# Optimization experiments

Hardware: AMD Instinct MI355X
Metric: run time of the kernel (lower is better)

Reference implementation:

```python
import jax, jax.numpy as jnp
import numpy as np

B, H, W, C = 16, 64, 64, 256
NH = 8          # num_heads
WS = 8          # window size (8,8) from shift=2
HID = 1024      # mlp hidden = 4*C
EPS = 1e-5


def _rel_index():
    # relative_position_index exactly as in the torch module (meshgrid 'ij')
    ch = np.arange(WS)
    coords = np.stack(np.meshgrid(ch, ch, indexing='ij'))          # (2, WS, WS)
    flat = coords.reshape(2, -1)                                    # (2, N)
    rel = flat[:, :, None] - flat[:, None, :]                       # (2, N, N)
    rel = rel.transpose(1, 2, 0).astype(np.int64)                   # (N, N, 2)
    rel[..., 0] += WS - 1
    rel[..., 1] += WS - 1
    rel[..., 0] *= 2 * WS - 1
    return jnp.asarray(rel.sum(-1))                                 # (N, N)


def _ln(x, w, b):
    m = x.mean(-1, keepdims=True)
    v = jnp.mean((x - m) ** 2, axis=-1, keepdims=True)
    return (x - m) / jnp.sqrt(v + EPS) * w + b


def setup_inputs() -> dict:
    key = jax.random.key(0)
    ks = jax.random.split(key, 16)
    std = 0.02
    n_bias = (2 * WS - 1) * (2 * WS - 1)  # 225
    return {
        'x': jax.random.normal(ks[0], (B, H * W, C), jnp.float32),
        'norm1_w': jnp.ones((C,), jnp.float32),
        'norm1_b': jnp.zeros((C,), jnp.float32),
        'qkv_w': jax.random.normal(ks[1], (3 * C, C), jnp.float32) * std,
        'qkv_b': jnp.zeros((3 * C,), jnp.float32),
        'rel_bias': jax.random.normal(ks[2], (n_bias, NH), jnp.float32) * std,
        'proj_w': jax.random.normal(ks[3], (C, C), jnp.float32) * std,
        'proj_b': jnp.zeros((C,), jnp.float32),
        'norm2_w': jnp.ones((C,), jnp.float32),
        'norm2_b': jnp.zeros((C,), jnp.float32),
        'fc1_w': jax.random.normal(ks[4], (HID, C), jnp.float32) * std,
        'fc1_b': jnp.zeros((HID,), jnp.float32),
        'dw_w': jax.random.normal(ks[5], (3, 3, 1, HID), jnp.float32) * std,  # HWIO depthwise
        'dw_b': jnp.zeros((HID,), jnp.float32),
        'fc2_w': jax.random.normal(ks[6], (C, HID), jnp.float32) * std,
        'fc2_b': jnp.zeros((C,), jnp.float32),
    }


def reference(x, norm1_w, norm1_b, qkv_w, qkv_b, rel_bias, proj_w, proj_b,
              norm2_w, norm2_b, fc1_w, fc1_b, dw_w, dw_b, fc2_w, fc2_b):
    S = (H // WS) * (W // WS)   # num windows = 64
    N = WS * WS                 # tokens per window = 64
    shortcut = x
    h = _ln(x, norm1_w, norm1_b).reshape(B, H, W, C)
    # window partition -> (B, S, N, C), then permute to (B, N, S, C)
    hw = (h.reshape(B, H // WS, WS, W // WS, WS, C)
            .transpose(0, 1, 3, 2, 4, 5)
            .reshape(B, S, N, C))
    xw = hw.transpose(0, 2, 1, 3)            # (B, N, S, C)
    # qkv over flattened (N*S) tokens; heads split the S*C feature dim
    xf = xw.reshape(B, N * S, C)
    qkv = xf @ qkv_w.T + qkv_b               # (B, N*S, 3C)
    qkv = qkv.reshape(B, N, 3, NH, S * C // NH).transpose(2, 0, 3, 1, 4)
    q, k, v = qkv[0], qkv[1], qkv[2]         # (B, NH, N, S*C/NH)
    scale = (C // NH) ** -0.5
    attn = jnp.einsum('bhnd,bhmd->bhnm', q, k) * scale   # (B, NH, N, N)
    idx = _rel_index()
    bias = rel_bias[idx.reshape(-1)].reshape(N, N, NH).transpose(2, 0, 1)
    attn = jax.nn.softmax(attn + bias[None], axis=-1)
    out = jnp.einsum('bhnm,bhmd->bhnd', attn, v)         # (B, NH, N, S*C/NH)
    out = out.transpose(0, 2, 1, 3).reshape(B, N * S, C)
    out = (out @ proj_w.T + proj_b).reshape(B, N, S, C).transpose(0, 2, 1, 3)  # (B,S,N,C)
    # window reverse -> (B, H*W, C)
    xr = (out.reshape(B, H // WS, W // WS, WS, WS, C)
             .transpose(0, 1, 3, 2, 4, 5)
             .reshape(B, H * W, C))
    x = shortcut + xr
    # conv-based MLP (eval mode, dropout = identity)
    y = _ln(x, norm2_w, norm2_b).reshape(B, H, H, C)      # NHWC
    y = jnp.einsum('bhwc,oc->bhwo', y, fc1_w) + fc1_b     # 1x1 conv
    y = jax.lax.conv_general_dilated(
        y, dw_w, (1, 1), 'SAME',
        dimension_numbers=('NHWC', 'HWIO', 'NHWC'),
        feature_group_count=HID) + dw_b
    y = jax.nn.gelu(y, approximate=False)
    y = jnp.einsum('bhwo,co->bhwc', y, fc2_w) + fc2_b     # 1x1 conv
    return x + y.reshape(B, H * W, C)
```

## Files before the change

kernel.cpp:

```cpp
#include <hip/hip_runtime.h>
#include <hip/hip_bf16.h>
#include <cstdint>
#include <cstddef>

#define B_     16
#define HW_    4096
#define C_     256
#define NH_    8
#define S_     64
#define N_     64
#define C3_    768
#define HID_   1024
#define DHEAD_ 2048
#define EPS_   1e-5f

using u16 = unsigned short;
using u32 = unsigned int;

typedef __attribute__((ext_vector_type(8))) short bf16x8;
typedef __attribute__((ext_vector_type(4))) float f32x4;

__device__ __forceinline__ float bf2f(u16 u) {
  union { float f; u32 i; } x; x.i = ((u32)u) << 16; return x.f;
}
__device__ __forceinline__ u16 f2bf(float f) {
  union { float f; u32 i; } x; x.f = f;
  u32 r = (x.i + 0x7FFFu + ((x.i >> 16) & 1u)) >> 16;
  return (u16)r;
}

__device__ __forceinline__ void gload_lds16(const u16* g, u16* l) {
  __builtin_amdgcn_global_load_lds(
      (const __attribute__((address_space(1))) unsigned int*)g,
      (__attribute__((address_space(3))) unsigned int*)l, 16, 0, 0);
}

__launch_bounds__(256)
__global__ void pack_w_kernel(const float* __restrict__ W, u16* __restrict__ out,
                              int K, int kshift) {
  int g = blockIdx.x * 256 + threadIdx.x;
  int lane = g & 63;
  int pk = g >> 6;
  int cb = pk >> kshift;
  int kb = pk & ((1 << kshift) - 1);
  int j = cb * 16 + (lane & 15);
  int k = kb * 32 + ((lane >> 4) << 3);
  const float* src = W + (size_t)j * K + k;
  float4 a = ((const float4*)src)[0];
  float4 b = ((const float4*)src)[1];
  ushort4 lo = {f2bf(a.x), f2bf(a.y), f2bf(a.z), f2bf(a.w)};
  ushort4 hi = {f2bf(b.x), f2bf(b.y), f2bf(b.z), f2bf(b.w)};
  ushort4* dst = (ushort4*)(out + (size_t)g * 8);
  dst[0] = lo;
  dst[1] = hi;
}

__launch_bounds__(256)
__global__ void ln_kernel(const float* __restrict__ in, const float* __restrict__ w,
                          const float* __restrict__ bias, u16* __restrict__ out,
                          int b_base) {
  int wave = threadIdx.x >> 6;
  int lane = threadIdx.x & 63;
  int t = blockIdx.x * 4 + wave;
  int b = b_base + (t >> 12);
  int r = t & 4095;
  int n = r >> 6, s = r & 63;
  int hw = (((s >> 3) << 3) + (n >> 3)) * 64 + ((s & 7) << 3) + (n & 7);
  size_t src_row = ((size_t)b << 12) + hw;
  float4 v = ((const float4*)(in + src_row * C_))[lane];
  float sum = v.x + v.y + v.z + v.w;
#pragma unroll
  for (int off = 32; off; off >>= 1) sum += __shfl_xor(sum, off);
  float mean = sum * (1.0f / C_);
  float4 d = {v.x - mean, v.y - mean, v.z - mean, v.w - mean};
  float ss = d.x * d.x + d.y * d.y + d.z * d.z + d.w * d.w;
#pragma unroll
  for (int off = 32; off; off >>= 1) ss += __shfl_xor(ss, off);
  float rstd = rsqrtf(ss * (1.0f / C_) + EPS_);
  float4 w4 = ((const float4*)w)[lane];
  float4 b4 = ((const float4*)bias)[lane];
  ushort4 o;
  o.x = f2bf(d.x * rstd * w4.x + b4.x);
  o.y = f2bf(d.y * rstd * w4.y + b4.y);
  o.z = f2bf(d.z * rstd * w4.z + b4.z);
  o.w = f2bf(d.w * rstd * w4.w + b4.w);
  ((ushort4*)(out + (size_t)t * C_))[lane] = o;
}

template<int K_, int J_, int EPI>
__launch_bounds__(256)
__global__ void gemm_mfma(const u16* __restrict__ A, const u16* __restrict__ wpk,
                          const float* __restrict__ bias, u16* __restrict__ outB,
                          float* __restrict__ outF, const float* __restrict__ res,
                          int m_base, u16* __restrict__ qb, u16* __restrict__ kb,
                          u16* __restrict__ vt) {
  constexpr int NT = K_ / 64;
  __shared__ u16 As[2][128 * 64];
  int tid = threadIdx.x;
  int wid = tid >> 6, lane = tid & 63;
  int n0 = blockIdx.x * 128;
  int m0 = blockIdx.y * 128;
  int wr = wid >> 1, wc = wid & 1;
  f32x4 acc[4][4] = {};
  int srow8 = lane >> 3, sslot = lane & 7;

#define ASTAGE(buf, t)                                                         \
  {                                                                            \
    int k0g = (t) * 64;                                                        \
    int cbb = ((sslot ^ srow8) << 4);                                          \
    _Pragma("unroll")                                                          \
    for (int r = 0; r < 4; ++r) {                                              \
      int row = wid * 32 + r * 8 + srow8;                                      \
      gload_lds16(A + (size_t)(m0 + row) * K_ + k0g + (cbb >> 1),              \
                  &As[buf][(wid * 32 + r * 8) * 64]);                          \
    }                                                                          \
  }

  ASTAGE(0, 0);
  asm volatile("s_waitcnt vmcnt(0)" ::: "memory");
  __builtin_amdgcn_sched_barrier(0);
  __builtin_amdgcn_s_barrier();
  __builtin_amdgcn_sched_barrier(0);

  for (int t = 0; t < NT; ++t) {
    bf16x8 bfr[8];
#pragma unroll
    for (int kk = 0; kk < 2; ++kk)
#pragma unroll
      for (int nf = 0; nf < 4; ++nf)
        bfr[kk * 4 + nf] = *(const bf16x8*)&wpk[
            ((size_t)(((n0 >> 4) + wc * 4 + nf) * (K_ / 32) + (t * 2 + kk)) * 64 + lane) * 8];
    if (t + 1 < NT) ASTAGE((t + 1) & 1, t + 1);
    const u16* as = As[t & 1];
#pragma unroll
    for (int kk = 0; kk < 2; ++kk) {
      bf16x8 afr[4];
#pragma unroll
      for (int mf = 0; mf < 4; ++mf) {
        int ra = wr * 64 + mf * 16 + (lane & 15);
        int cbb = (((kk * 4 + (lane >> 4)) ^ (ra & 7)) << 4);
        afr[mf] = *(const bf16x8*)&as[ra * 64 + (cbb >> 1)];
      }
#pragma unroll
      for (int mf = 0; mf < 4; ++mf)
#pragma unroll
        for (int nf = 0; nf < 4; ++nf)
          acc[mf][nf] = __builtin_amdgcn_mfma_f32_16x16x32_bf16(afr[mf], bfr[kk * 4 + nf], acc[mf][nf], 0, 0, 0);
    }
    asm volatile("s_waitcnt vmcnt(0)" ::: "memory");
    __builtin_amdgcn_sched_barrier(0);
    __builtin_amdgcn_s_barrier();
    __builtin_amdgcn_sched_barrier(0);
  }
#undef ASTAGE

#pragma unroll
  for (int nf = 0; nf < 4; ++nf) {
    int col = n0 + wc * 64 + nf * 16 + (lane & 15);
    float bv = bias[col];
#pragma unroll
    for (int mf = 0; mf < 4; ++mf) {
#pragma unroll
      for (int j = 0; j < 4; ++j) {
        int m = m0 + wr * 64 + mf * 16 + (lane >> 4) * 4 + j;
        float v = acc[mf][nf][j] + bv;
        if (EPI == 0) {
          outB[(size_t)m * J_ + col] = f2bf(v);
        } else if (EPI == 2) {
          size_t o = (size_t)(m_base + m) * C_ + col;
          outF[o] += v;
        } else {
          int b_rel = m >> 12, nn = (m >> 6) & 63, s = m & 63;
          int f = s * 768 + col;
          int part = f >> 14, hh = (f >> 11) & 7, d = f & 2047;
          u16 val = f2bf(v);
          size_t bh = (size_t)b_rel * 8 + hh;
          if (part == 0)      qb[(bh * 64 + nn) * 2048 + d] = val;
          else if (part == 1) kb[(bh * 64 + nn) * 2048 + d] = val;
          else                vt[(bh * 2048 + d) * 64 + nn] = val;
        }
      }
    }
  }
}

__launch_bounds__(256)
__global__ void proj_ln_fused(const u16* __restrict__ A, const u16* __restrict__ wpk,
                              const float* __restrict__ bias, const float* __restrict__ res,
                              float* __restrict__ outF, const float* __restrict__ ln_w,
                              const float* __restrict__ ln_b, u16* __restrict__ h2,
                              int m_base) {
  __shared__ u16 As[2][64 * 64];
  __shared__ float red[64][8];
  int tid = threadIdx.x;
  int wid = tid >> 6, lane = tid & 63;
  int m0 = blockIdx.x * 64;
  f32x4 acc[4][4] = {};
  int srow8 = lane >> 3, sslot = lane & 7;

#define PSTAGE(buf, t)                                                         \
  {                                                                            \
    int k0g = (t) * 64;                                                        \
    int cbb = ((sslot ^ srow8) << 4);                                          \
    _Pragma("unroll")                                                          \
    for (int r = 0; r < 2; ++r) {                                              \
      int row = wid * 16 + r * 8 + srow8;                                      \
      gload_lds16(A + (size_t)(m0 + row) * 256 + k0g + (cbb >> 1),             \
                  &As[buf][(wid * 16 + r * 8) * 64]);                          \
    }                                                                          \
  }

  PSTAGE(0, 0);
  asm volatile("s_waitcnt vmcnt(0)" ::: "memory");
  __builtin_amdgcn_sched_barrier(0);
  __builtin_amdgcn_s_barrier();
  __builtin_amdgcn_sched_barrier(0);

#pragma unroll
  for (int t = 0; t < 4; ++t) {
    bf16x8 bfr[8];
#pragma unroll
    for (int kk = 0; kk < 2; ++kk)
#pragma unroll
      for (int nf = 0; nf < 4; ++nf)
        bfr[kk * 4 + nf] = *(const bf16x8*)&wpk[
            ((size_t)((wid * 4 + nf) * 8 + (t * 2 + kk)) * 64 + lane) * 8];
    if (t + 1 < 4) PSTAGE((t + 1) & 1, t + 1);
    const u16* as = As[t & 1];
#pragma unroll
    for (int kk = 0; kk < 2; ++kk) {
      bf16x8 afr[4];
#pragma unroll
      for (int mf = 0; mf < 4; ++mf) {
        int ra = mf * 16 + (lane & 15);
        int cbb = (((kk * 4 + (lane >> 4)) ^ (ra & 7)) << 4);
        afr[mf] = *(const bf16x8*)&as[ra * 64 + (cbb >> 1)];
      }
#pragma unroll
      for (int mf = 0; mf < 4; ++mf)
#pragma unroll
        for (int nf = 0; nf < 4; ++nf)
          acc[mf][nf] = __builtin_amdgcn_mfma_f32_16x16x32_bf16(afr[mf], bfr[kk * 4 + nf], acc[mf][nf], 0, 0, 0);
    }
    asm volatile("s_waitcnt vmcnt(0)" ::: "memory");
    __builtin_amdgcn_sched_barrier(0);
    __builtin_amdgcn_s_barrier();
    __builtin_amdgcn_sched_barrier(0);
  }
#undef PSTAGE

#pragma unroll
  for (int mf = 0; mf < 4; ++mf) {
#pragma unroll
    for (int j = 0; j < 4; ++j) {
      int m = m0 + mf * 16 + (lane >> 4) * 4 + j;
      int gm = m_base + m;
      int b = gm >> 12, nn = (gm >> 6) & 63, s = gm & 63;
      int hw = (((s >> 3) << 3) + (nn >> 3)) * 64 + ((s & 7) << 3) + (nn & 7);
      size_t rowo = (((size_t)b << 12) + hw) * C_;
      float s1 = 0.f, s2 = 0.f;
#pragma unroll
      for (int nf = 0; nf < 4; ++nf) {
        int col = wid * 64 + nf * 16 + (lane & 15);
        float v = acc[mf][nf][j] + bias[col] + res[rowo + col];
        acc[mf][nf][j] = v;
        outF[rowo + col] = v;
        s1 += v; s2 += v * v;
      }
#pragma unroll
      for (int off = 1; off < 16; off <<= 1) {
        s1 += __shfl_xor(s1, off);
        s2 += __shfl_xor(s2, off);
      }
      if ((lane & 15) == 0) {
        int rr = mf * 16 + (lane >> 4) * 4 + j;
        red[rr][wid * 2] = s1;
        red[rr][wid * 2 + 1] = s2;
      }
    }
  }
  __syncthreads();

#pragma unroll
  for (int mf = 0; mf < 4; ++mf) {
#pragma unroll
    for (int j = 0; j < 4; ++j) {
      int rr = mf * 16 + (lane >> 4) * 4 + j;
      float sum = red[rr][0] + red[rr][2] + red[rr][4] + red[rr][6];
      float ssq = red[rr][1] + red[rr][3] + red[rr][5] + red[rr][7];
      float mean = sum * (1.0f / C_);
      float var = ssq * (1.0f / C_) - mean * mean;
      float rstd = rsqrtf(var + EPS_);
      int m = m0 + rr;
      int b_rel = m >> 12, nn = (m >> 6) & 63, s = m & 63;
      int hw = (((s >> 3) << 3) + (nn >> 3)) * 64 + ((s & 7) << 3) + (nn & 7);
      size_t ho = (((size_t)b_rel << 12) + hw) * C_;
#pragma unroll
      for (int nf = 0; nf < 4; ++nf) {
        int col = wid * 64 + nf * 16 + (lane & 15);
        float nv = (acc[mf][nf][j] - mean) * rstd * ln_w[col] + ln_b[col];
        h2[ho + col] = f2bf(nv);
      }
    }
  }
}

__launch_bounds__(256)
__global__ void attn_mfma(const u16* __restrict__ qb, const u16* __restrict__ kb,
                          const u16* __restrict__ vt, const float* __restrict__ rel_bias,
                          u16* __restrict__ outp) {
  __shared__ u16 bufA[4096];
  __shared__ u16 bufB[4096];
  int bh = blockIdx.x;
  int h = bh & 7;
  int b_rel = bh >> 3;
  int tid = threadIdx.x;
  int w = tid >> 6, lane = tid & 63;
  int l3 = lane >> 3, l7 = lane & 7;
  const u16* qg = qb + (size_t)bh * 64 * 2048;
  const u16* kg = kb + (size_t)bh * 64 * 2048;
  const u16* vg = vt + (size_t)bh * 2048 * 64;

  f32x4 acc[4] = {};
  for (int k0 = 0; k0 < 2048; k0 += 64) {
#pragma unroll
    for (int r = 0; r < 2; ++r) {
      int row = w * 16 + r * 8 + l3;
      int sc = (l7 ^ (row & 7)) * 8;
      gload_lds16(qg + (size_t)row * 2048 + k0 + sc, &bufA[(w * 16 + r * 8) * 64]);
      gload_lds16(kg + (size_t)row * 2048 + k0 + sc, &bufB[(w * 16 + r * 8) * 64]);
    }
    __syncthreads();
    int rowq = w * 16 + (lane & 15);
#pragma unroll
    for (int ks = 0; ks < 2; ++ks) {
      bf16x8 aq = *(const bf16x8*)&bufA[rowq * 64 + (((ks * 4 + (lane >> 4)) ^ (rowq & 7)) << 3)];
#pragma unroll
      for (int cf = 0; cf < 4; ++cf) {
        int m = cf * 16 + (lane & 15);
        bf16x8 bk = *(const bf16x8*)&bufB[m * 64 + (((ks * 4 + (lane >> 4)) ^ (m & 7)) << 3)];
        acc[cf] = __builtin_amdgcn_mfma_f32_16x16x32_bf16(aq, bk, acc[cf], 0, 0, 0);
      }
    }
    __syncthreads();
  }

  const float scale = 0.17677669529663688f;
#pragma unroll
  for (int j = 0; j < 4; ++j) {
    int r = w * 16 + (lane >> 4) * 4 + j;
    int i1 = r >> 3, j1 = r & 7;
    float v[4];
#pragma unroll
    for (int cf = 0; cf < 4; ++cf) {
      int c = cf * 16 + (lane & 15);
      int idx = (i1 - (c >> 3) + 7) * 15 + (j1 - (c & 7) + 7);
      v[cf] = acc[cf][j] * scale + rel_bias[idx * NH_ + h];
    }
    float mx = fmaxf(fmaxf(v[0], v[1]), fmaxf(v[2], v[3]));
#pragma unroll
    for (int off = 8; off; off >>= 1) mx = fmaxf(mx, __shfl_xor(mx, off));
    float sm = 0.f;
#pragma unroll
    for (int cf = 0; cf < 4; ++cf) { v[cf] = __expf(v[cf] - mx); sm += v[cf]; }
#pragma unroll
    for (int off = 8; off; off >>= 1) sm += __shfl_xor(sm, off);
    float inv = 1.0f / sm;
#pragma unroll
    for (int cf = 0; cf < 4; ++cf) {
      int c = cf * 16 + (lane & 15);
      bufA[r * 64 + (c ^ ((r & 7) << 3))] = f2bf(v[cf] * inv);
    }
  }
  __syncthreads();

  bf16x8 pa[2];
  {
    int n = w * 16 + (lane & 15);
#pragma unroll
    for (int ks = 0; ks < 2; ++ks)
      pa[ks] = *(const bf16x8*)&bufA[n * 64 + ((ks * 32 + (lane >> 4) * 8) ^ ((n & 7) << 3))];
  }

  for (int d0 = 0; d0 < 2048; d0 += 64) {
#pragma unroll
    for (int r = 0; r < 2; ++r) {
      int drow = w * 16 + r * 8 + l3;
      int sc = (l7 ^ (drow & 7)) * 8;
      gload_lds16(vg + (size_t)(d0 + drow) * 64 + sc, &bufB[(w * 16 + r * 8) * 64]);
    }
    __syncthreads();
    f32x4 o[4] = {};
#pragma unroll
    for (int ks = 0; ks < 2; ++ks)
#pragma unroll
      for (int cf = 0; cf < 4; ++cf) {
        int d = cf * 16 + (lane & 15);
        bf16x8 bv = *(const bf16x8*)&bufB[d * 64 + (((ks * 4 + (lane >> 4)) ^ (d & 7)) << 3)];
        o[cf] = __builtin_amdgcn_mfma_f32_16x16x32_bf16(pa[ks], bv, o[cf], 0, 0, 0);
      }
#pragma unroll
    for (int cf = 0; cf < 4; ++cf) {
      int f = h * 2048 + d0 + cf * 16 + (lane & 15);
      int s = f >> 8, c = f & 255;
#pragma unroll
      for (int j = 0; j < 4; ++j) {
        int n = w * 16 + (lane >> 4) * 4 + j;
        outp[(((size_t)b_rel * 64 + n) * 64 + s) * 256 + c] = f2bf(o[cf][j]);
      }
    }
    __syncthreads();
  }
}

__launch_bounds__(256)
__global__ void dwconv_gelu(const u16* __restrict__ y1, const float* __restrict__ dw_w,
                            const float* __restrict__ dw_b, u16* __restrict__ y2) {
  int bid = blockIdx.x;
  int wt = bid & 31, ht = (bid >> 5) & 15, b = bid >> 9;
  int h0 = ht * 4, w0 = wt * 2;
  int c0 = threadIdx.x * 4;

  float4 wv[9];
#pragma unroll
  for (int i = 0; i < 9; ++i) wv[i] = *(const float4*)&dw_w[i * HID_ + c0];

  ushort4 in[6][4];
#pragma unroll
  for (int ii = 0; ii < 6; ++ii) {
    int hh = h0 + ii - 1;
#pragma unroll
    for (int jj = 0; jj < 4; ++jj) {
      int ww = w0 + jj - 1;
      if ((unsigned)hh < 64u && (unsigned)ww < 64u)
        in[ii][jj] = *(const ushort4*)(y1 + ((size_t)((b << 12) + hh * 64 + ww)) * HID_ + c0);
      else
        in[ii][jj] = ushort4{0, 0, 0, 0};
    }
  }

  float4 bv = *(const float4*)&dw_b[c0];
  float4 acc[4][2];
#pragma unroll
  for (int i = 0; i < 4; ++i)
#pragma unroll
    for (int j = 0; j < 2; ++j) acc[i][j] = bv;

#pragma unroll
  for (int ii = 0; ii < 6; ++ii) {
#pragma unroll
    for (int jj = 0; jj < 4; ++jj) {
      ushort4 u = in[ii][jj];
      float4 f = {bf2f(u.x), bf2f(u.y), bf2f(u.z), bf2f(u.w)};
#pragma unroll
      for (int kh = 0; kh < 3; ++kh) {
        int i = ii - kh;
        if (i < 0 || i > 3) continue;
#pragma unroll
        for (int kw = 0; kw < 3; ++kw) {
          int j = jj - kw;
          if (j < 0 || j > 1) continue;
          float4 w4 = wv[kh * 3 + kw];
          acc[i][j].x += f.x * w4.x;
          acc[i][j].y += f.y * w4.y;
          acc[i][j].z += f.z * w4.z;
          acc[i][j].w += f.w * w4.w;
        }
      }
    }
  }

  const float k = 0.70710678118654752f;
#pragma unroll
  for (int i = 0; i < 4; ++i) {
#pragma unroll
    for (int j = 0; j < 2; ++j) {
      float4 a = acc[i][j];
      ushort4 o;
      o.x = f2bf(0.5f * a.x * (1.0f + erff(a.x * k)));
      o.y = f2bf(0.5f * a.y * (1.0f + erff(a.y * k)));
      o.z = f2bf(0.5f * a.z * (1.0f + erff(a.z * k)));
      o.w = f2bf(0.5f * a.w * (1.0f + erff(a.w * k)));
      *(ushort4*)(y2 + ((size_t)((b << 12) + (h0 + i) * 64 + (w0 + j))) * HID_ + c0) = o;
    }
  }
}

extern "C" void kernel_launch(void* const* d_in, const int* in_sizes, int n_in,
                              void* d_out, int out_size, void* d_ws, size_t ws_size,
                              hipStream_t stream) {
  const float* x       = (const float*)d_in[0];
  const float* norm1_w = (const float*)d_in[1];
  const float* norm1_b = (const float*)d_in[2];
  const float* qkv_w   = (const float*)d_in[3];
  const float* qkv_b   = (const float*)d_in[4];
  const float* rel_b   = (const float*)d_in[5];
  const float* proj_w  = (const float*)d_in[6];
  const float* proj_b  = (const float*)d_in[7];
  const float* norm2_w = (const float*)d_in[8];
  const float* norm2_b = (const float*)d_in[9];
  const float* fc1_w   = (const float*)d_in[10];
  const float* fc1_b   = (const float*)d_in[11];
  const float* dw_w    = (const float*)d_in[12];
  const float* dw_b    = (const float*)d_in[13];
  const float* fc2_w   = (const float*)d_in[14];
  const float* fc2_b   = (const float*)d_in[15];
  float* out = (float*)d_out;
  char* ws = (char*)d_ws;

  u16* wq = (u16*)(ws);
  u16* wp = wq + 768 * 256;
  u16* w1 = wp + 256 * 256;
  u16* w2 = w1 + 1024 * 256;
  pack_w_kernel<<<768 * 256 / 8 / 256, 256, 0, stream>>>(qkv_w, wq, 256, 3);
  pack_w_kernel<<<256 * 256 / 8 / 256, 256, 0, stream>>>(proj_w, wp, 256, 3);
  pack_w_kernel<<<1024 * 256 / 8 / 256, 256, 0, stream>>>(fc1_w, w1, 256, 3);
  pack_w_kernel<<<256 * 1024 / 8 / 256, 256, 0, stream>>>(fc2_w, w2, 1024, 5);

  const size_t MBy = (size_t)1 << 20;
  char* cws = ws + 2 * MBy;
  int G = 1;
  for (int g = 16; g >= 1; g >>= 1) {
    if (2 * MBy + (size_t)(18 * g) * MBy <= ws_size) { G = g; break; }
  }
  const size_t gm = (size_t)G * MBy;
  u16* h1c    = (u16*)(cws);
  u16* qbuf   = (u16*)(cws + 2 * gm);
  u16* kbuf   = (u16*)(cws + 4 * gm);
  u16* vtbuf  = (u16*)(cws + 6 * gm);
  u16* attnoc = (u16*)(cws + 8 * gm);
  u16* h2c    = (u16*)(cws);
  u16* y1c    = (u16*)(cws + 2 * gm);
  u16* y2c    = (u16*)(cws + 10 * gm);

  const int Mloc = G * 4096;
  for (int b0 = 0; b0 < B_; b0 += G) {
    ln_kernel<<<Mloc / 4, 256, 0, stream>>>(x, norm1_w, norm1_b, h1c, b0);
    gemm_mfma<256, 768, 3><<<dim3(6, Mloc / 128), 256, 0, stream>>>(
        h1c, wq, qkv_b, nullptr, nullptr, nullptr, 0, qbuf, kbuf, vtbuf);
    attn_mfma<<<G * 8, 256, 0, stream>>>(qbuf, kbuf, vtbuf, rel_b, attnoc);
    proj_ln_fused<<<Mloc / 64, 256, 0, stream>>>(
        attnoc, wp, proj_b, x, out, norm2_w, norm2_b, h2c, b0 * 4096);
    gemm_mfma<256, 1024, 0><<<dim3(8, Mloc / 128), 256, 0, stream>>>(
        h2c, w1, fc1_b, y1c, nullptr, nullptr, 0, nullptr, nullptr, nullptr);
    dwconv_gelu<<<Mloc / 8, 256, 0, stream>>>(y1c, dw_w, dw_b, y2c);
    gemm_mfma<1024, 256, 2><<<dim3(2, Mloc / 128), 256, 0, stream>>>(
        y2c, w2, fc2_b, nullptr, out, nullptr, b0 * 4096, nullptr, nullptr, nullptr);
  }
}
```

Baseline: 533.0 us.

## Fuse depthwise conv+GELU with fc2 GEMM via shared-memory tile

Replaces the separate depthwise-conv/GELU kernel and the fc2 GEMM with one kernel. Each block computes GELU(dwconv) for a 8x4 pixel tile into a swizzled 64KB LDS buffer, then runs the fc2 MFMA over it and accumulates into the output. This removes the y2 round trip through global memory and one launch, and the smaller workspace need allows larger batch groups. In exchange it adds 9x redundant global reads of y1 (no halo reuse), B-operand reads straight from global, only 32 rows per block, and low occupancy because of the large LDS footprint.

```diff
diff --git a/kernel.cpp b/kernel.cpp
--- a/kernel.cpp
+++ b/kernel.cpp
@@ -91,7 +91,6 @@
 __launch_bounds__(256)
 __global__ void gemm_mfma(const u16* __restrict__ A, const u16* __restrict__ wpk,
                           const float* __restrict__ bias, u16* __restrict__ outB,
-                          float* __restrict__ outF, const float* __restrict__ res,
                           int m_base, u16* __restrict__ qb, u16* __restrict__ kb,
                           u16* __restrict__ vt) {
   constexpr int NT = K_ / 64;
@@ -166,9 +165,6 @@
         float v = acc[mf][nf][j] + bv;
         if (EPI == 0) {
           outB[(size_t)m * J_ + col] = f2bf(v);
-        } else if (EPI == 2) {
-          size_t o = (size_t)(m_base + m) * C_ + col;
-          outF[o] += v;
         } else {
           int b_rel = m >> 12, nn = (m >> 6) & 63, s = m & 63;
           int f = s * 768 + col;
@@ -414,74 +410,103 @@
 }
 
 __launch_bounds__(256)
-__global__ void dwconv_gelu(const u16* __restrict__ y1, const float* __restrict__ dw_w,
-                            const float* __restrict__ dw_b, u16* __restrict__ y2) {
+__global__ void mlp2_fused(const u16* __restrict__ y1, const float* __restrict__ dw_w,
+                           const float* __restrict__ dw_b, const u16* __restrict__ wpk,
+                           const float* __restrict__ fc2_b, float* __restrict__ outF,
+                           int b0) {
+  __shared__ u16 y2t[32 * 1024];
   int bid = blockIdx.x;
-  int wt = bid & 31, ht = (bid >> 5) & 15, b = bid >> 9;
-  int h0 = ht * 4, w0 = wt * 2;
-  int c0 = threadIdx.x * 4;
-
-  float4 wv[9];
-#pragma unroll
-  for (int i = 0; i < 9; ++i) wv[i] = *(const float4*)&dw_w[i * HID_ + c0];
-
-  ushort4 in[6][4];
-#pragma unroll
-  for (int ii = 0; ii < 6; ++ii) {
-    int hh = h0 + ii - 1;
-#pragma unroll
-    for (int jj = 0; jj < 4; ++jj) {
-      int ww = w0 + jj - 1;
-      if ((unsigned)hh < 64u && (unsigned)ww < 64u)
-        in[ii][jj] = *(const ushort4*)(y1 + ((size_t)((b << 12) + hh * 64 + ww)) * HID_ + c0);
-      else
-        in[ii][jj] = ushort4{0, 0, 0, 0};
-    }
-  }
-
-  float4 bv = *(const float4*)&dw_b[c0];
-  float4 acc[4][2];
-#pragma unroll
-  for (int i = 0; i < 4; ++i)
-#pragma unroll
-    for (int j = 0; j < 2; ++j) acc[i][j] = bv;
-
-#pragma unroll
-  for (int ii = 0; ii < 6; ++ii) {
-#pragma unroll
-    for (int jj = 0; jj < 4; ++jj) {
-      ushort4 u = in[ii][jj];
-      float4 f = {bf2f(u.x), bf2f(u.y), bf2f(u.z), bf2f(u.w)};
-#pragma unroll
-      for (int kh = 0; kh < 3; ++kh) {
-        int i = ii - kh;
-        if (i < 0 || i > 3) continue;
-#pragma unroll
-        for (int kw = 0; kw < 3; ++kw) {
-          int j = jj - kw;
-          if (j < 0 || j > 1) continue;
-          float4 w4 = wv[kh * 3 + kw];
-          acc[i][j].x += f.x * w4.x;
-          acc[i][j].y += f.y * w4.y;
-          acc[i][j].z += f.z * w4.z;
-          acc[i][j].w += f.w * w4.w;
-        }
-      }
-    }
-  }
-
-  const float k = 0.70710678118654752f;
-#pragma unroll
-  for (int i = 0; i < 4; ++i) {
-#pragma unroll
-    for (int j = 0; j < 2; ++j) {
-      float4 a = acc[i][j];
-      ushort4 o;
-      o.x = f2bf(0.5f * a.x * (1.0f + erff(a.x * k)));
-      o.y = f2bf(0.5f * a.y * (1.0f + erff(a.y * k)));
-      o.z = f2bf(0.5f * a.z * (1.0f + erff(a.z * k)));
-      o.w = f2bf(0.5f * a.w * (1.0f + erff(a.w * k)));
-      *(ushort4*)(y2 + ((size_t)((b << 12) + (h0 + i) * 64 + (w0 + j))) * HID_ + c0) = o;
+  int tw = bid & 15, th = (bid >> 4) & 7, b_rel = bid >> 7;
+  int h0 = th * 8, w0 = tw * 4;
+  int tid = threadIdx.x;
+  int g = tid & 127;
+  int set = tid >> 7;
+  int c8 = g * 8;
+
+  float4 wv[9][2];
+#pragma unroll
+  for (int i = 0; i < 9; ++i) {
+    wv[i][0] = *(const float4*)&dw_w[i * HID_ + c8];
+    wv[i][1] = *(const float4*)&dw_w[i * HID_ + c8 + 4];
+  }
+  float4 bv0 = *(const float4*)&dw_b[c8];
+  float4 bv1 = *(const float4*)&dw_b[c8 + 4];
+
+  const size_t img = (size_t)b_rel << 12;
+#pragma unroll
+  for (int i = 0; i < 16; ++i) {
+    int px = set * 16 + i;
+    int ph = px >> 2, pw = px & 3;
+    float4 a0 = bv0, a1 = bv1;
+#pragma unroll
+    for (int kh = 0; kh < 3; ++kh) {
+      int hh = h0 + ph + kh - 1;
+      if (hh < 0 || hh > 63) continue;
+#pragma unroll
+      for (int kw = 0; kw < 3; ++kw) {
+        int ww = w0 + pw + kw - 1;
+        if (ww < 0 || ww > 63) continue;
+        const u16* src = y1 + (img + hh * 64 + ww) * HID_ + c8;
+        ushort4 u0 = ((const ushort4*)src)[0];
+        ushort4 u1 = ((const ushort4*)src)[1];
+        float4 wa = wv[kh * 3 + kw][0], wb = wv[kh * 3 + kw][1];
+        a0.x += bf2f(u0.x) * wa.x; a0.y += bf2f(u0.y) * wa.y;
+        a0.z += bf2f(u0.z) * wa.z; a0.w += bf2f(u0.w) * wa.w;
+        a1.x += bf2f(u1.x) * wb.x; a1.y += bf2f(u1.y) * wb.y;
+        a1.z += bf2f(u1.z) * wb.z; a1.w += bf2f(u1.w) * wb.w;
+      }
+    }
+    const float kG = 0.70710678118654752f;
+    ushort4 o0, o1;
+    o0.x = f2bf(0.5f * a0.x * (1.0f + erff(a0.x * kG)));
+    o0.y = f2bf(0.5f * a0.y * (1.0f + erff(a0.y * kG)));
+    o0.z = f2bf(0.5f * a0.z * (1.0f + erff(a0.z * kG)));
+    o0.w = f2bf(0.5f * a0.w * (1.0f + erff(a0.w * kG)));
+    o1.x = f2bf(0.5f * a1.x * (1.0f + erff(a1.x * kG)));
+    o1.y = f2bf(0.5f * a1.y * (1.0f + erff(a1.y * kG)));
+    o1.z = f2bf(0.5f * a1.z * (1.0f + erff(a1.z * kG)));
+    o1.w = f2bf(0.5f * a1.w * (1.0f + erff(a1.w * kG)));
+    ushort4* dst = (ushort4*)&y2t[px * 1024 + ((g ^ (px & 7)) << 3)];
+    dst[0] = o0;
+    dst[1] = o1;
+  }
+  __syncthreads();
+
+  int wvid = tid >> 6, lane = tid & 63;
+  f32x4 acc[2][4] = {};
+#pragma unroll
+  for (int kb32 = 0; kb32 < 32; ++kb32) {
+    bf16x8 afr[2], bfr[4];
+#pragma unroll
+    for (int mf = 0; mf < 2; ++mf) {
+      int row = mf * 16 + (lane & 15);
+      int unit = kb32 * 4 + (lane >> 4);
+      afr[mf] = *(const bf16x8*)&y2t[row * 1024 + ((unit ^ (row & 7)) << 3)];
+    }
+#pragma unroll
+    for (int nf = 0; nf < 4; ++nf)
+      bfr[nf] = *(const bf16x8*)&wpk[
+          ((size_t)((wvid * 4 + nf) * 32 + kb32) * 64 + lane) * 8];
+#pragma unroll
+    for (int mf = 0; mf < 2; ++mf)
+#pragma unroll
+      for (int nf = 0; nf < 4; ++nf)
+        acc[mf][nf] = __builtin_amdgcn_mfma_f32_16x16x32_bf16(afr[mf], bfr[nf], acc[mf][nf], 0, 0, 0);
+  }
+
+#pragma unroll
+  for (int nf = 0; nf < 4; ++nf) {
+    int col = wvid * 64 + nf * 16 + (lane & 15);
+    float bb = fc2_b[col];
+#pragma unroll
+    for (int mf = 0; mf < 2; ++mf) {
+#pragma unroll
+      for (int j = 0; j < 4; ++j) {
+        int px = mf * 16 + (lane >> 4) * 4 + j;
+        int ph = px >> 2, pw = px & 3;
+        size_t o = (((size_t)(b0 + b_rel) << 12) + (h0 + ph) * 64 + (w0 + pw)) * C_ + col;
+        outF[o] += acc[mf][nf][j] + bb;
+      }
     }
   }
 }
@@ -521,7 +546,7 @@
   char* cws = ws + 2 * MBy;
   int G = 1;
   for (int g = 16; g >= 1; g >>= 1) {
-    if (2 * MBy + (size_t)(18 * g) * MBy <= ws_size) { G = g; break; }
+    if (2 * MBy + (size_t)(10 * g) * MBy <= ws_size) { G = g; break; }
   }
   const size_t gm = (size_t)G * MBy;
   u16* h1c    = (u16*)(cws);
@@ -531,20 +556,17 @@
   u16* attnoc = (u16*)(cws + 8 * gm);
   u16* h2c    = (u16*)(cws);
   u16* y1c    = (u16*)(cws + 2 * gm);
-  u16* y2c    = (u16*)(cws + 10 * gm);
 
   const int Mloc = G * 4096;
   for (int b0 = 0; b0 < B_; b0 += G) {
     ln_kernel<<<Mloc / 4, 256, 0, stream>>>(x, norm1_w, norm1_b, h1c, b0);
     gemm_mfma<256, 768, 3><<<dim3(6, Mloc / 128), 256, 0, stream>>>(
-        h1c, wq, qkv_b, nullptr, nullptr, nullptr, 0, qbuf, kbuf, vtbuf);
+        h1c, wq, qkv_b, nullptr, 0, qbuf, kbuf, vtbuf);
     attn_mfma<<<G * 8, 256, 0, stream>>>(qbuf, kbuf, vtbuf, rel_b, attnoc);
     proj_ln_fused<<<Mloc / 64, 256, 0, stream>>>(
         attnoc, wp, proj_b, x, out, norm2_w, norm2_b, h2c, b0 * 4096);
     gemm_mfma<256, 1024, 0><<<dim3(8, Mloc / 128), 256, 0, stream>>>(
-        h2c, w1, fc1_b, y1c, nullptr, nullptr, 0, nullptr, nullptr, nullptr);
-    dwconv_gelu<<<Mloc / 8, 256, 0, stream>>>(y1c, dw_w, dw_b, y2c);
-    gemm_mfma<1024, 256, 2><<<dim3(2, Mloc / 128), 256, 0, stream>>>(
-        y2c, w2, fc2_b, nullptr, out, nullptr, b0 * 4096, nullptr, nullptr, nullptr);
-  }
-}
+        h2c, w1, fc1_b, y1c, 0, nullptr, nullptr, nullptr);
+    mlp2_fused<<<G * 128, 256, 0, stream>>>(y1c, dw_w, dw_b, w2, fc2_b, out, b0);
+  }
+}
```

After: 531.9 us. Within noise of the previous version (-0.2%).
